# Optimization experiments

Hardware: AMD Instinct MI355X
Metric: run time of the kernel (lower is better)

The kernel has to match this reference:

```python
import jax, jax.numpy as jnp
import numpy as np

B, S, D, H = 4, 1024, 512, 8
EPS = 1e-5


def _cx(x):
    # [..., 2] float -> complex
    return jax.lax.complex(x[..., 0], x[..., 1])


def setup_inputs() -> dict:
    key = jax.random.key(0)
    ks = jax.random.split(key, 9)
    f = lambda k, sh: jax.random.normal(k, sh, dtype=jnp.float32)
    inp = {
        "q": f(ks[0], (B, S, D, 2)),
        "k": f(ks[1], (B, S, D, 2)),
        "v": f(ks[2], (B, S, D, 2)),
        "Wq": f(ks[3], (D, D, 2)) * 0.02,
        "bq": f(ks[4], (D, 2)) * 0.02,
        "Wk": f(ks[5], (D, D, 2)) * 0.02,
        "bk": f(ks[6], (D, 2)) * 0.02,
        "Wv": f(ks[7], (D, D, 2)) * 0.02,
        "bv": f(ks[8], (D, 2)) * 0.02,
        "gamma_r": jnp.ones((D,), jnp.float32),
        "beta_r": jnp.zeros((D,), jnp.float32),
        "gamma_i": jnp.ones((D,), jnp.float32),
        "beta_i": jnp.zeros((D,), jnp.float32),
        "n_heads": H,
    }
    return inp


def _layernorm(x, g, b):
    # torch LayerNorm: biased variance, eps inside sqrt
    mu = jnp.mean(x, axis=-1, keepdims=True)
    var = jnp.mean((x - mu) ** 2, axis=-1, keepdims=True)
    return (x - mu) / jnp.sqrt(var + EPS) * g + b


def reference(q, k, v, Wq, bq, Wk, bk, Wv, bv, gamma_r, beta_r, gamma_i, beta_i, n_heads):
    qc, kc, vc = _cx(q), _cx(k), _cx(v)
    # complex linear: x @ W^T + b
    Q = jnp.einsum("bsd,ed->bse", qc, _cx(Wq)) + _cx(bq)
    K = jnp.einsum("bsd,ed->bse", kc, _cx(Wk)) + _cx(bk)
    V = jnp.einsum("bsd,ed->bse", vc, _cx(Wv)) + _cx(bv)
    b, s, d = qc.shape
    dh = d // n_heads
    Qh = Q.reshape(b, s, n_heads, dh)
    Kh = K.reshape(b, s, n_heads, dh)
    Vh = V.reshape(b, s, n_heads, dh)
    # complex scores [b,h,q,k], scaled by sqrt(dh)
    scores = jnp.einsum("bqhd,bkhd->bhqk", Qh, Kh) / jnp.sqrt(jnp.float32(dh))
    # original: softmax over view_as_real dim=-2 == key axis, real & imag independently
    attn = jax.lax.complex(jax.nn.softmax(scores.real, axis=-1),
                           jax.nn.softmax(scores.imag, axis=-1))
    # (dropout is identity in eval mode)
    out = jnp.einsum("bhqk,bkhd->bqhd", attn, Vh).reshape(b, s, d)
    out = out + qc  # residual
    out_r = _layernorm(out.real, gamma_r, beta_r)
    out_i = _layernorm(out.imag, gamma_i, beta_i)
    return jnp.stack([out_r, out_i], axis=-1)  # [B,S,D,2]
```

## Files before the change

### kernel.cpp

```cpp
#include <hip/hip_runtime.h>
#include <math.h>

#define BB  4
#define SS  1024
#define DD  512
#define HH  8
#define DHD 64
#define PL  2097152
#define WPL 262144

constexpr float LN_EPS = 1e-5f;

using half4 = __attribute__((ext_vector_type(4))) _Float16;
using half8 = __attribute__((ext_vector_type(8))) _Float16;
using f32x4 = __attribute__((ext_vector_type(4))) float;

__device__ __forceinline__ half8 negh(half8 a) {
    union { half8 h; unsigned int u[4]; } t;
    t.h = a;
    #pragma unroll
    for (int i = 0; i < 4; ++i) t.u[i] ^= 0x80008000u;
    return t.h;
}
__device__ __forceinline__ half8 ldh64(const unsigned short* p, int row, int col) {
    return *(const half8*)(p + row * 64 + (col ^ ((row & 7) << 3)));
}
__device__ __forceinline__ unsigned int cvtpk(float a, float b) {
    union { decltype(__builtin_amdgcn_cvt_pkrtz(0.f, 0.f)) v; unsigned int u; } t;
    t.v = __builtin_amdgcn_cvt_pkrtz(a, b);
    return t.u;
}
__device__ __forceinline__ float ex2(float x) { return __builtin_amdgcn_exp2f(x); }
#define MFMA16(acc, a, b) acc = __builtin_amdgcn_mfma_f32_16x16x32_f16(a, b, acc, 0, 0, 0)

__global__ __launch_bounds__(256)
void cvt_kernel(const float2* __restrict__ s0, const float2* __restrict__ s1,
                const float2* __restrict__ s2, unsigned short* __restrict__ dst,
                int planeElems) {
    const int z = blockIdx.y;
    const float2* src = z == 0 ? s0 : (z == 1 ? s1 : s2);
    unsigned short* base = dst + (size_t)z * 2 * planeElems;
    const int idx = (blockIdx.x * 256 + threadIdx.x) * 2;
    float4 t = *(const float4*)(src + idx);
    const int m = idx >> 9;
    const int d = idx & 511;
    const int ob = (((m >> 7) << 3) + (d >> 6)) * 8192 + ((m & 127) << 6) + (d & 63);
    union { _Float16 h[2]; unsigned int u; } r, i;
    r.h[0] = (_Float16)t.x; r.h[1] = (_Float16)t.z;
    i.h[0] = (_Float16)t.y; i.h[1] = (_Float16)t.w;
    *(unsigned int*)(base + ob) = r.u;
    *(unsigned int*)(base + planeElems + ob) = i.u;
}

__global__ __launch_bounds__(256, 2)
void proj_kernel(const unsigned short* __restrict__ XP,
                 const unsigned short* __restrict__ WP,
                 const float2* __restrict__ bq, const float2* __restrict__ bk,
                 const float2* __restrict__ bv,
                 unsigned short* __restrict__ QG, unsigned short* __restrict__ KG,
                 unsigned short* __restrict__ VG) {
    const unsigned short* XR = XP + (size_t)blockIdx.z * 2 * PL;
    const unsigned short* XI = XR + PL;
    const unsigned short* WRp = WP + (size_t)blockIdx.z * 2 * WPL;
    const unsigned short* WIp = WRp + WPL;
    const float2* bias; unsigned short* outP;
    if (blockIdx.z == 0)      { bias = bq; outP = QG; }
    else if (blockIdx.z == 1) { bias = bk; outP = KG; }
    else                      { bias = bv; outP = VG; }
    const bool isV = (blockIdx.z == 2);

    __shared__ __align__(16) unsigned short Xs[2][128 * 64];
    __shared__ __align__(16) unsigned short Ws[2][128 * 64];

    const int tid  = threadIdx.x;
    const int w    = tid >> 6;
    const int lane = tid & 63;
    const int quad = lane >> 4;
    const int l15  = lane & 15;
    const int wm   = w >> 1;
    const int we   = w & 1;
    const int m0   = blockIdx.x * 128;
    const int e0   = blockIdx.y * 128;

    const int srow = lane >> 3;
    const int sg   = lane & 7;
    const unsigned short* gplane;
    unsigned short* lb;
    int row0;
    if (w == 0)      { gplane = XR;  row0 = m0; lb = &Xs[0][0]; }
    else if (w == 1) { gplane = XI;  row0 = m0; lb = &Xs[1][0]; }
    else if (w == 2) { gplane = WRp; row0 = e0; lb = &Ws[0][0]; }
    else             { gplane = WIp; row0 = e0; lb = &Ws[1][0]; }
    const unsigned short* gs = gplane + (size_t)row0 * DD + srow * 64 + ((sg ^ srow) << 3);

    f32x4 Sr[4][4], Si[4][4];
    #pragma unroll
    for (int a = 0; a < 4; ++a)
        #pragma unroll
        for (int c = 0; c < 4; ++c) { Sr[a][c] = (f32x4)0.f; Si[a][c] = (f32x4)0.f; }

    for (int s = 0; s < 8; ++s) {
        if (s) __syncthreads();
        const unsigned short* _g = gs + (size_t)s * 8192;
        #pragma unroll
        for (int j = 0; j < 16; ++j)
            __builtin_amdgcn_global_load_lds(
                (const __attribute__((address_space(1))) void*)(_g + j * 512),
                (__attribute__((address_space(3))) void*)(lb + j * 512),
                16, 0, 0);
        __syncthreads();

        #pragma unroll
        for (int kc = 0; kc < 2; ++kc) {
            const int dl = kc * 32 + quad * 8;
            half8 xr[4], xi[4];
            #pragma unroll
            for (int mf = 0; mf < 4; ++mf) {
                const int mr = wm * 64 + mf * 16 + l15;
                xr[mf] = ldh64(Xs[0], mr, dl);
                xi[mf] = ldh64(Xs[1], mr, dl);
            }
            #pragma unroll
            for (int ef = 0; ef < 4; ++ef) {
                const int er = we * 64 + ef * 16 + l15;
                half8 wr  = ldh64(Ws[0], er, dl);
                half8 wi  = ldh64(Ws[1], er, dl);
                half8 wmi = negh(wi);
                #pragma unroll
                for (int mf = 0; mf < 4; ++mf) {
                    MFMA16(Sr[mf][ef], xr[mf], wr);
                    MFMA16(Sr[mf][ef], xi[mf], wmi);
                    MFMA16(Si[mf][ef], xr[mf], wi);
                    MFMA16(Si[mf][ef], xi[mf], wr);
                }
            }
        }
    }

    #pragma unroll
    for (int ef = 0; ef < 4; ++ef) {
        const int eg  = e0 + we * 64 + ef * 16 + l15;
        const int hh  = eg >> 6;
        const int col = eg & 63;
        float2 bb = bias[eg];
        #pragma unroll
        for (int mf = 0; mf < 4; ++mf) {
            #pragma unroll
            for (int reg = 0; reg < 4; ++reg) {
                int m = m0 + wm * 64 + mf * 16 + quad * 4 + reg;
                int bidx = m >> 10;
                int sidx = m & 1023;
                int bh = bidx * HH + hh;
                union { _Float16 h; unsigned short u; } cr, ci;
                cr.h = (_Float16)(Sr[mf][ef][reg] + bb.x);
                ci.h = (_Float16)(Si[mf][ef][reg] + bb.y);
                size_t o = isV ? ((size_t)bh * DHD + col) * SS + sidx
                               : ((size_t)bh * SS + sidx) * DHD + col;
                outP[0 * PL + o] = cr.u;
                outP[1 * PL + o] = ci.u;
            }
        }
    }
}

#define AWID 72
__global__ __launch_bounds__(256, 2)
void attn_kernel(const unsigned short* __restrict__ QG, const unsigned short* __restrict__ KG,
                 const unsigned short* __restrict__ VG,
                 unsigned short* __restrict__ ObR, unsigned short* __restrict__ ObI) {
    __shared__ __align__(16) unsigned short Ks[2][2][64 * 64];
    __shared__ __align__(16) unsigned short Vt[2][64 * 64];
    __shared__ __align__(16) unsigned short Ps[2][64 * AWID];
    __shared__ float lbuf[2][2][64];

    const int n   = blockIdx.x;
    const int bh  = (n & 7) * 4 + (n >> 7);
    const int q0  = ((n >> 3) & 15) * 64;
    const int b   = bh >> 3;
    const int h   = bh & 7;

    const int tid  = threadIdx.x;
    const int w    = tid >> 6;
    const int lane = tid & 63;
    const int quad = lane >> 4;
    const int l15  = lane & 15;
    const int sw   = w & 1;
    const int tw   = w >> 1;

    const int srow = lane >> 3;
    const int sg   = lane & 7;
    const bool isK = (w < 2);
    const unsigned short* bpK = nullptr;
    const unsigned short* bpV = nullptr;
    unsigned short* ldV = nullptr;
    if (isK) {
        bpK = KG + (size_t)w * PL + (size_t)bh * SS * DHD + srow * DHD + ((sg ^ srow) << 3);
    } else {
        bpV = VG + (size_t)(w - 2) * PL + (size_t)bh * DHD * SS + srow * SS + ((sg ^ srow) << 3);
        ldV = &Vt[w - 2][0];
    }

#define GLD(SRC, DST) __builtin_amdgcn_global_load_lds( \
        (const __attribute__((address_space(1))) void*)(SRC), \
        (__attribute__((address_space(3))) void*)(DST), 16, 0, 0)

    if (isK) {
        unsigned short* ld = &Ks[0][w][0];
        #pragma unroll
        for (int j = 0; j < 8; ++j) GLD(bpK + j * 8 * DHD, ld + j * 512);
    }

    half8 qfr[2][2], qfi[2][2], qfmi[2][2];
    #pragma unroll
    for (int qt = 0; qt < 2; ++qt)
        #pragma unroll
        for (int kc = 0; kc < 2; ++kc) {
            size_t qa = ((size_t)bh * SS + q0 + sw * 32 + qt * 16 + l15) * DHD + kc * 32 + quad * 8;
            qfr[qt][kc]  = *(const half8*)(QG + qa);
            qfi[qt][kc]  = *(const half8*)(QG + PL + qa);
            qfmi[qt][kc] = negh(qfi[qt][kc]);
        }

    f32x4 acc[2][2][4];
    #pragma unroll
    for (int qt = 0; qt < 2; ++qt)
        #pragma unroll
        for (int dt = 0; dt < 2; ++dt)
            #pragma unroll
            for (int p = 0; p < 4; ++p) acc[qt][dt][p] = (f32x4)0.f;
    float lacc[2][2] = {{0.f, 0.f}, {0.f, 0.f}};

    constexpr float EC = 0.18033688011112042f;

    __syncthreads();

    const unsigned short* Kr_c = &Ks[0][0][0];
    const unsigned short* Ki_c = &Ks[0][1][0];
    const unsigned short* Kr_n = &Ks[1][0][0];
    const unsigned short* Ki_n = &Ks[1][1][0];
    unsigned short* kst_nxt = isK ? &Ks[1][w][0] : nullptr;
    unsigned short* kst_alt = isK ? &Ks[0][w][0] : nullptr;

    for (int t = 0; t < 16; ++t) {
        if (isK) {
            if (t < 15) {
                const unsigned short* g = bpK + (size_t)(t + 1) * 64 * DHD;
                #pragma unroll
                for (int j = 0; j < 8; ++j) GLD(g + j * 8 * DHD, kst_nxt + j * 512);
            }
        } else {
            const unsigned short* g = bpV + (size_t)t * 64;
            #pragma unroll
            for (int j = 0; j < 8; ++j) GLD(g + j * 8 * SS, ldV + j * 512);
        }

        f32x4 Sr[2][2], Si[2][2];
        #pragma unroll
        for (int a = 0; a < 2; ++a)
            #pragma unroll
            for (int c = 0; c < 2; ++c) { Sr[a][c] = (f32x4)0.f; Si[a][c] = (f32x4)0.f; }
        #pragma unroll
        for (int kc = 0; kc < 2; ++kc) {
            const int dl = kc * 32 + quad * 8;
            #pragma unroll
            for (int kt2 = 0; kt2 < 2; ++kt2) {
                const int krow = tw * 32 + kt2 * 16 + l15;
                half8 akr = ldh64(Kr_c, krow, dl);
                half8 aki = ldh64(Ki_c, krow, dl);
                #pragma unroll
                for (int qt = 0; qt < 2; ++qt) {
                    MFMA16(Sr[kt2][qt], akr, qfr[qt][kc]);
                    MFMA16(Sr[kt2][qt], aki, qfmi[qt][kc]);
                    MFMA16(Si[kt2][qt], aki, qfr[qt][kc]);
                    MFMA16(Si[kt2][qt], akr, qfi[qt][kc]);
                }
            }
        }

        #pragma unroll
        for (int kt2 = 0; kt2 < 2; ++kt2)
            #pragma unroll
            for (int qt = 0; qt < 2; ++qt) {
                float er0 = ex2(Sr[kt2][qt][0] * EC), er1 = ex2(Sr[kt2][qt][1] * EC);
                float er2 = ex2(Sr[kt2][qt][2] * EC), er3 = ex2(Sr[kt2][qt][3] * EC);
                float ei0 = ex2(Si[kt2][qt][0] * EC), ei1 = ex2(Si[kt2][qt][1] * EC);
                float ei2 = ex2(Si[kt2][qt][2] * EC), ei3 = ex2(Si[kt2][qt][3] * EC);
                lacc[qt][0] += (er0 + er1) + (er2 + er3);
                lacc[qt][1] += (ei0 + ei1) + (ei2 + ei3);
                const int qrow = sw * 32 + qt * 16 + l15;
                const int kcol = tw * 32 + kt2 * 16 + quad * 4;
                uint2 pr, pi;
                pr.x = cvtpk(er0, er1); pr.y = cvtpk(er2, er3);
                pi.x = cvtpk(ei0, ei1); pi.y = cvtpk(ei2, ei3);
                *(uint2*)&Ps[0][qrow * AWID + kcol] = pr;
                *(uint2*)&Ps[1][qrow * AWID + kcol] = pi;
            }
        __syncthreads();

        #pragma unroll
        for (int kc = 0; kc < 2; ++kc) {
            half8 ap[2][2];
            #pragma unroll
            for (int qt = 0; qt < 2; ++qt) {
                const int qrow = sw * 32 + qt * 16 + l15;
                ap[qt][0] = *(const half8*)&Ps[0][qrow * AWID + kc * 32 + quad * 8];
                ap[qt][1] = *(const half8*)&Ps[1][qrow * AWID + kc * 32 + quad * 8];
            }
            #pragma unroll
            for (int dt = 0; dt < 2; ++dt) {
                const int drow = tw * 32 + dt * 16 + l15;
                half8 bvr = ldh64(Vt[0], drow, kc * 32 + quad * 8);
                half8 bvi = ldh64(Vt[1], drow, kc * 32 + quad * 8);
                #pragma unroll
                for (int qt = 0; qt < 2; ++qt) {
                    MFMA16(acc[qt][dt][0], ap[qt][0], bvr);
                    MFMA16(acc[qt][dt][1], ap[qt][0], bvi);
                    MFMA16(acc[qt][dt][2], ap[qt][1], bvr);
                    MFMA16(acc[qt][dt][3], ap[qt][1], bvi);
                }
            }
        }
        __syncthreads();

        const unsigned short* tr;
        tr = Kr_c; Kr_c = Kr_n; Kr_n = tr;
        tr = Ki_c; Ki_c = Ki_n; Ki_n = tr;
        unsigned short* ts = kst_nxt; kst_nxt = kst_alt; kst_alt = ts;
    }
#undef GLD

    #pragma unroll
    for (int qt = 0; qt < 2; ++qt)
        #pragma unroll
        for (int p = 0; p < 2; ++p) {
            float v = lacc[qt][p];
            v += __shfl_xor(v, 16);
            v += __shfl_xor(v, 32);
            if (lane < 16) lbuf[p][tw][sw * 32 + qt * 16 + lane] = v;
        }
    __syncthreads();

    #pragma unroll
    for (int qt = 0; qt < 2; ++qt)
        #pragma unroll
        for (int reg = 0; reg < 4; ++reg) {
            const int qloc = sw * 32 + qt * 16 + quad * 4 + reg;
            const float ir = 1.f / (lbuf[0][0][qloc] + lbuf[0][1][qloc]);
            const float ii = 1.f / (lbuf[1][0][qloc] + lbuf[1][1][qloc]);
            #pragma unroll
            for (int dt = 0; dt < 2; ++dt) {
                const int d = tw * 32 + dt * 16 + l15;
                union { _Float16 h; unsigned short u; } cr, ci;
                cr.h = (_Float16)(acc[qt][dt][0][reg] * ir - acc[qt][dt][3][reg] * ii);
                ci.h = (_Float16)(acc[qt][dt][1][reg] * ir + acc[qt][dt][2][reg] * ii);
                size_t o = ((size_t)b * SS + q0 + qloc) * DD + h * DHD + d;
                ObR[o] = cr.u;
                ObI[o] = ci.u;
            }
        }
}

__global__ __launch_bounds__(256)
void ln_kernel(const unsigned short* __restrict__ OrP, const unsigned short* __restrict__ OiP,
               const float2* __restrict__ Qin,
               const float* __restrict__ gr, const float* __restrict__ br,
               const float* __restrict__ gi, const float* __restrict__ bi,
               float2* __restrict__ out) {
    const int row = blockIdx.x;
    const int tid = threadIdx.x;
    const size_t base = (size_t)row * DD;
    const int e0 = 2 * tid, e1 = 2 * tid + 1;

    union { unsigned int u; _Float16 h[2]; } tr, ti;
    tr.u = *(const unsigned int*)(OrP + base + e0);
    ti.u = *(const unsigned int*)(OiP + base + e0);
    float2 r0 = Qin[base + e0];
    float2 r1 = Qin[base + e1];
    float xr0 = (float)tr.h[0] + r0.x;
    float xr1 = (float)tr.h[1] + r1.x;
    float xi0 = (float)ti.h[0] + r0.y;
    float xi1 = (float)ti.h[1] + r1.y;

    float sr = xr0 + xr1;
    float si = xi0 + xi1;
    float qr = xr0 * xr0 + xr1 * xr1;
    float qi = xi0 * xi0 + xi1 * xi1;
    #pragma unroll
    for (int off = 32; off > 0; off >>= 1) {
        sr += __shfl_down(sr, off);
        si += __shfl_down(si, off);
        qr += __shfl_down(qr, off);
        qi += __shfl_down(qi, off);
    }
    __shared__ float red[4][4];
    __shared__ float stat[4];
    int lane = tid & 63, wid = tid >> 6;
    if (lane == 0) { red[wid][0] = sr; red[wid][1] = si; red[wid][2] = qr; red[wid][3] = qi; }
    __syncthreads();
    if (tid == 0) {
        sr = red[0][0] + red[1][0] + red[2][0] + red[3][0];
        si = red[0][1] + red[1][1] + red[2][1] + red[3][1];
        qr = red[0][2] + red[1][2] + red[2][2] + red[3][2];
        qi = red[0][3] + red[1][3] + red[2][3] + red[3][3];
        float mur = sr * (1.f / DD), mui = si * (1.f / DD);
        float vr = qr * (1.f / DD) - mur * mur;
        float vi = qi * (1.f / DD) - mui * mui;
        stat[0] = mur; stat[1] = mui;
        stat[2] = rsqrtf(vr + LN_EPS); stat[3] = rsqrtf(vi + LN_EPS);
    }
    __syncthreads();
    float mur = stat[0], mui = stat[1], rsr = stat[2], rsi = stat[3];
    out[base + e0] = make_float2((xr0 - mur) * rsr * gr[e0] + br[e0],
                                 (xi0 - mui) * rsi * gi[e0] + bi[e0]);
    out[base + e1] = make_float2((xr1 - mur) * rsr * gr[e1] + br[e1],
                                 (xi1 - mui) * rsi * gi[e1] + bi[e1]);
}

extern "C" void kernel_launch(void* const* d_in, const int* in_sizes, int n_in,
                              void* d_out, int out_size, void* d_ws, size_t ws_size,
                              hipStream_t stream) {
    const float2* q  = (const float2*)d_in[0];
    const float2* k  = (const float2*)d_in[1];
    const float2* v  = (const float2*)d_in[2];
    const float2* Wq = (const float2*)d_in[3];
    const float2* bq = (const float2*)d_in[4];
    const float2* Wk = (const float2*)d_in[5];
    const float2* bk = (const float2*)d_in[6];
    const float2* Wv = (const float2*)d_in[7];
    const float2* bv = (const float2*)d_in[8];
    const float*  gr = (const float*)d_in[9];
    const float*  br = (const float*)d_in[10];
    const float*  gi = (const float*)d_in[11];
    const float*  bi = (const float*)d_in[12];

    unsigned short* XP  = (unsigned short*)d_ws;
    unsigned short* WP  = XP + (size_t)6 * PL;
    unsigned short* QG  = WP + (size_t)6 * WPL;
    unsigned short* KG  = QG + (size_t)2 * PL;
    unsigned short* VG  = KG + (size_t)2 * PL;
    unsigned short* ObR = VG + (size_t)2 * PL;
    unsigned short* ObI = ObR + (size_t)PL;

    cvt_kernel<<<dim3(4096, 3), 256, 0, stream>>>(q, k, v, XP, PL);
    cvt_kernel<<<dim3(512, 3), 256, 0, stream>>>(Wq, Wk, Wv, WP, WPL);
    proj_kernel<<<dim3(32, 4, 3), 256, 0, stream>>>(XP, WP, bq, bk, bv, QG, KG, VG);
    attn_kernel<<<dim3(512), 256, 0, stream>>>(QG, KG, VG, ObR, ObI);
    ln_kernel<<<dim3(BB * SS), 256, 0, stream>>>(ObR, ObI, q, gr, br, gi, bi, (float2*)d_out);
}
```

Baseline: 205.2 us.

## Double-buffer projection LDS tiles and relax attention barriers with split waitcnts

The projection GEMM now loads K in 32-wide half-stages into two LDS buffers, so the global-to-LDS load of the next stage overlaps the MFMAs on the current one. This replaces the old load, full sync, compute pattern, and adds a new swizzled 32-column addressing helper. In the attention kernel, the __syncthreads calls are replaced by explicit s_waitcnt plus s_barrier, waiting on vector memory only where needed (isK), so in-flight loads are not drained too early. Both changes add more barriers per K step and rely on hand-written waitcnt correctness.

Result: slower. 209.3 us (+2.0%).

```diff
diff --git a/kernel.cpp b/kernel.cpp
--- a/kernel.cpp
+++ b/kernel.cpp
@@ -24,6 +24,11 @@
 }
 __device__ __forceinline__ half8 ldh64(const unsigned short* p, int row, int col) {
     return *(const half8*)(p + row * 64 + (col ^ ((row & 7) << 3)));
+}
+__device__ __forceinline__ half8 ldh32(const unsigned short* p, int r, int g2) {
+    const int R = r >> 1;
+    const int G = ((r & 1) << 2) | g2;
+    return *(const half8*)(p + R * 64 + ((G ^ (R & 7)) << 3));
 }
 __device__ __forceinline__ unsigned int cvtpk(float a, float b) {
     union { decltype(__builtin_amdgcn_cvt_pkrtz(0.f, 0.f)) v; unsigned int u; } t;
@@ -69,8 +74,8 @@
     else                      { bias = bv; outP = VG; }
     const bool isV = (blockIdx.z == 2);
 
-    __shared__ __align__(16) unsigned short Xs[2][128 * 64];
-    __shared__ __align__(16) unsigned short Ws[2][128 * 64];
+    __shared__ __align__(16) unsigned short Xs[2][2][64 * 64];
+    __shared__ __align__(16) unsigned short Ws[2][2][64 * 64];
 
     const int tid  = threadIdx.x;
     const int w    = tid >> 6;
@@ -82,16 +87,28 @@
     const int m0   = blockIdx.x * 128;
     const int e0   = blockIdx.y * 128;
 
-    const int srow = lane >> 3;
-    const int sg   = lane & 7;
+    const int srow8 = lane >> 3;
+    const int G     = (lane & 7) ^ srow8;
+    const int rl    = srow8 * 2 + (G >> 2);
+    const int g2s   = G & 3;
+
     const unsigned short* gplane;
-    unsigned short* lb;
+    unsigned short *lb0, *lb1;
     int row0;
-    if (w == 0)      { gplane = XR;  row0 = m0; lb = &Xs[0][0]; }
-    else if (w == 1) { gplane = XI;  row0 = m0; lb = &Xs[1][0]; }
-    else if (w == 2) { gplane = WRp; row0 = e0; lb = &Ws[0][0]; }
-    else             { gplane = WIp; row0 = e0; lb = &Ws[1][0]; }
-    const unsigned short* gs = gplane + (size_t)row0 * DD + srow * 64 + ((sg ^ srow) << 3);
+    if (w == 0)      { gplane = XR;  row0 = m0; lb0 = &Xs[0][0][0]; lb1 = &Xs[1][0][0]; }
+    else if (w == 1) { gplane = XI;  row0 = m0; lb0 = &Xs[0][1][0]; lb1 = &Xs[1][1][0]; }
+    else if (w == 2) { gplane = WRp; row0 = e0; lb0 = &Ws[0][0][0]; lb1 = &Ws[1][0][0]; }
+    else             { gplane = WIp; row0 = e0; lb0 = &Ws[0][1][0]; lb1 = &Ws[1][1][0]; }
+    const unsigned short* gsrc = gplane + (size_t)row0 * DD + rl * 64 + g2s * 8;
+
+#define PSTAGE(S, LB) { \
+        const unsigned short* _g = gsrc + ((S) >> 1) * 8192 + ((S) & 1) * 32; \
+        _Pragma("unroll") \
+        for (int j = 0; j < 8; ++j) \
+            __builtin_amdgcn_global_load_lds( \
+                (const __attribute__((address_space(1))) void*)(_g + j * 1024), \
+                (__attribute__((address_space(3))) void*)((LB) + j * 512), \
+                16, 0, 0); }
 
     f32x4 Sr[4][4], Si[4][4];
     #pragma unroll
@@ -99,43 +116,44 @@
         #pragma unroll
         for (int c = 0; c < 4; ++c) { Sr[a][c] = (f32x4)0.f; Si[a][c] = (f32x4)0.f; }
 
-    for (int s = 0; s < 8; ++s) {
-        if (s) __syncthreads();
-        const unsigned short* _g = gs + (size_t)s * 8192;
-        #pragma unroll
-        for (int j = 0; j < 16; ++j)
-            __builtin_amdgcn_global_load_lds(
-                (const __attribute__((address_space(1))) void*)(_g + j * 512),
-                (__attribute__((address_space(3))) void*)(lb + j * 512),
-                16, 0, 0);
-        __syncthreads();
-
-        #pragma unroll
-        for (int kc = 0; kc < 2; ++kc) {
-            const int dl = kc * 32 + quad * 8;
-            half8 xr[4], xi[4];
+    PSTAGE(0, lb0);
+    __syncthreads();
+
+    for (int s = 0; s < 16; ++s) {
+        const int bs = s & 1;
+        if (s < 15) PSTAGE(s + 1, bs ? lb0 : lb1);
+
+        const unsigned short* xb0 = &Xs[bs][0][0];
+        const unsigned short* xb1 = &Xs[bs][1][0];
+        const unsigned short* wb0 = &Ws[bs][0][0];
+        const unsigned short* wb1 = &Ws[bs][1][0];
+
+        half8 xr[4], xi[4];
+        #pragma unroll
+        for (int mf = 0; mf < 4; ++mf) {
+            const int mr = wm * 64 + mf * 16 + l15;
+            xr[mf] = ldh32(xb0, mr, quad);
+            xi[mf] = ldh32(xb1, mr, quad);
+        }
+        #pragma unroll
+        for (int ef = 0; ef < 4; ++ef) {
+            const int er = we * 64 + ef * 16 + l15;
+            half8 wr  = ldh32(wb0, er, quad);
+            half8 wi  = ldh32(wb1, er, quad);
+            half8 wmi = negh(wi);
             #pragma unroll
             for (int mf = 0; mf < 4; ++mf) {
-                const int mr = wm * 64 + mf * 16 + l15;
-                xr[mf] = ldh64(Xs[0], mr, dl);
-                xi[mf] = ldh64(Xs[1], mr, dl);
-            }
-            #pragma unroll
-            for (int ef = 0; ef < 4; ++ef) {
-                const int er = we * 64 + ef * 16 + l15;
-                half8 wr  = ldh64(Ws[0], er, dl);
-                half8 wi  = ldh64(Ws[1], er, dl);
-                half8 wmi = negh(wi);
-                #pragma unroll
-                for (int mf = 0; mf < 4; ++mf) {
-                    MFMA16(Sr[mf][ef], xr[mf], wr);
-                    MFMA16(Sr[mf][ef], xi[mf], wmi);
-                    MFMA16(Si[mf][ef], xr[mf], wi);
-                    MFMA16(Si[mf][ef], xi[mf], wr);
-                }
-            }
-        }
-    }
+                MFMA16(Sr[mf][ef], xr[mf], wr);
+                MFMA16(Sr[mf][ef], xi[mf], wmi);
+                MFMA16(Si[mf][ef], xr[mf], wi);
+                MFMA16(Si[mf][ef], xi[mf], wr);
+            }
+        }
+        asm volatile("s_waitcnt vmcnt(0)" ::: "memory");
+        __builtin_amdgcn_s_barrier();
+        asm volatile("" ::: "memory");
+    }
+#undef PSTAGE
 
     #pragma unroll
     for (int ef = 0; ef < 4; ++ef) {
@@ -295,7 +313,11 @@
                 *(uint2*)&Ps[0][qrow * AWID + kcol] = pr;
                 *(uint2*)&Ps[1][qrow * AWID + kcol] = pi;
             }
-        __syncthreads();
+
+        asm volatile("s_waitcnt lgkmcnt(0)" ::: "memory");
+        if (!isK) asm volatile("s_waitcnt vmcnt(0)" ::: "memory");
+        __builtin_amdgcn_s_barrier();
+        asm volatile("" ::: "memory");
 
         #pragma unroll
         for (int kc = 0; kc < 2; ++kc) {
@@ -320,7 +342,10 @@
                 }
             }
         }
-        __syncthreads();
+
+        if (isK) asm volatile("s_waitcnt vmcnt(0)" ::: "memory");
+        __builtin_amdgcn_s_barrier();
+        asm volatile("" ::: "memory");
 
         const unsigned short* tr;
         tr = Kr_c; Kr_c = Kr_n; Kr_n = tr;
```

## Halve projection M-tile to raise occupancy and relax attention barrier waits

Applied to the files above, without the earlier changes.

The projection kernel now uses 64-row M tiles instead of 128, doubling the grid and lowering accumulator registers so launch bounds can allow three blocks per CU. The global-to-LDS loads are reassigned so one wave loads both X planes and two waves load the weight planes, with the fourth wave idle during loads. Separately, the attention loop replaces full __syncthreads with explicit lgkmcnt/vmcnt waits plus s_barrier, placing the vmcnt wait differently for K-loading waves so prefetch loads can stay in flight across the P·V phase. The smaller tile reduces per-block reuse of the weight tile, and the hand-placed waits risk ordering errors if the load roles are misread.

New measurement: 205.9 us. Within noise of the previous version (+0.4%).

```diff
diff --git a/kernel.cpp b/kernel.cpp
--- a/kernel.cpp
+++ b/kernel.cpp
@@ -52,7 +52,7 @@
     *(unsigned int*)(base + planeElems + ob) = i.u;
 }
 
-__global__ __launch_bounds__(256, 2)
+__global__ __launch_bounds__(256, 3)
 void proj_kernel(const unsigned short* __restrict__ XP,
                  const unsigned short* __restrict__ WP,
                  const float2* __restrict__ bq, const float2* __restrict__ bk,
@@ -69,7 +69,7 @@
     else                      { bias = bv; outP = VG; }
     const bool isV = (blockIdx.z == 2);
 
-    __shared__ __align__(16) unsigned short Xs[2][128 * 64];
+    __shared__ __align__(16) unsigned short Xs[2][64 * 64];
     __shared__ __align__(16) unsigned short Ws[2][128 * 64];
 
     const int tid  = threadIdx.x;
@@ -79,44 +79,55 @@
     const int l15  = lane & 15;
     const int wm   = w >> 1;
     const int we   = w & 1;
-    const int m0   = blockIdx.x * 128;
+    const int m0   = blockIdx.x * 64;
     const int e0   = blockIdx.y * 128;
 
-    const int srow = lane >> 3;
-    const int sg   = lane & 7;
-    const unsigned short* gplane;
-    unsigned short* lb;
-    int row0;
-    if (w == 0)      { gplane = XR;  row0 = m0; lb = &Xs[0][0]; }
-    else if (w == 1) { gplane = XI;  row0 = m0; lb = &Xs[1][0]; }
-    else if (w == 2) { gplane = WRp; row0 = e0; lb = &Ws[0][0]; }
-    else             { gplane = WIp; row0 = e0; lb = &Ws[1][0]; }
-    const unsigned short* gs = gplane + (size_t)row0 * DD + srow * 64 + ((sg ^ srow) << 3);
-
-    f32x4 Sr[4][4], Si[4][4];
-    #pragma unroll
-    for (int a = 0; a < 4; ++a)
+    const int srow8 = lane >> 3;
+    const int sg    = lane & 7;
+    const int swz   = ((sg ^ srow8) << 3);
+    const int xbase = ((m0 >> 7) << 16) + ((m0 & 127) << 6);
+    const int wbase = ((e0 >> 7) << 16);
+    const unsigned short* gsX  = XR  + xbase + srow8 * 64 + swz;
+    const unsigned short* gsW0 = WRp + wbase + srow8 * 64 + swz;
+    const unsigned short* gsW1 = WIp + wbase + srow8 * 64 + swz;
+
+#define GLD(SRC, DST) __builtin_amdgcn_global_load_lds( \
+        (const __attribute__((address_space(1))) void*)(SRC), \
+        (__attribute__((address_space(3))) void*)(DST), 16, 0, 0)
+
+    f32x4 Sr[2][4], Si[2][4];
+    #pragma unroll
+    for (int a = 0; a < 2; ++a)
         #pragma unroll
         for (int c = 0; c < 4; ++c) { Sr[a][c] = (f32x4)0.f; Si[a][c] = (f32x4)0.f; }
 
     for (int s = 0; s < 8; ++s) {
         if (s) __syncthreads();
-        const unsigned short* _g = gs + (size_t)s * 8192;
-        #pragma unroll
-        for (int j = 0; j < 16; ++j)
-            __builtin_amdgcn_global_load_lds(
-                (const __attribute__((address_space(1))) void*)(_g + j * 512),
-                (__attribute__((address_space(3))) void*)(lb + j * 512),
-                16, 0, 0);
+        if (w == 0) {
+            const unsigned short* g = gsX + s * 8192;
+            #pragma unroll
+            for (int jj = 0; jj < 16; ++jj)
+                GLD(g + (jj >> 3) * PL + (jj & 7) * 512, &Xs[jj >> 3][(jj & 7) * 512]);
+        } else if (w == 1) {
+            const unsigned short* g = gsW0 + s * 8192;
+            #pragma unroll
+            for (int jj = 0; jj < 16; ++jj)
+                GLD(g + jj * 512, &Ws[0][jj * 512]);
+        } else if (w == 2) {
+            const unsigned short* g = gsW1 + s * 8192;
+            #pragma unroll
+            for (int jj = 0; jj < 16; ++jj)
+                GLD(g + jj * 512, &Ws[1][jj * 512]);
+        }
         __syncthreads();
 
         #pragma unroll
         for (int kc = 0; kc < 2; ++kc) {
             const int dl = kc * 32 + quad * 8;
-            half8 xr[4], xi[4];
-            #pragma unroll
-            for (int mf = 0; mf < 4; ++mf) {
-                const int mr = wm * 64 + mf * 16 + l15;
+            half8 xr[2], xi[2];
+            #pragma unroll
+            for (int mf = 0; mf < 2; ++mf) {
+                const int mr = wm * 32 + mf * 16 + l15;
                 xr[mf] = ldh64(Xs[0], mr, dl);
                 xi[mf] = ldh64(Xs[1], mr, dl);
             }
@@ -127,7 +138,7 @@
                 half8 wi  = ldh64(Ws[1], er, dl);
                 half8 wmi = negh(wi);
                 #pragma unroll
-                for (int mf = 0; mf < 4; ++mf) {
+                for (int mf = 0; mf < 2; ++mf) {
                     MFMA16(Sr[mf][ef], xr[mf], wr);
                     MFMA16(Sr[mf][ef], xi[mf], wmi);
                     MFMA16(Si[mf][ef], xr[mf], wi);
@@ -136,6 +147,7 @@
             }
         }
     }
+#undef GLD
 
     #pragma unroll
     for (int ef = 0; ef < 4; ++ef) {
@@ -144,10 +156,10 @@
         const int col = eg & 63;
         float2 bb = bias[eg];
         #pragma unroll
-        for (int mf = 0; mf < 4; ++mf) {
+        for (int mf = 0; mf < 2; ++mf) {
             #pragma unroll
             for (int reg = 0; reg < 4; ++reg) {
-                int m = m0 + wm * 64 + mf * 16 + quad * 4 + reg;
+                int m = m0 + wm * 32 + mf * 16 + quad * 4 + reg;
                 int bidx = m >> 10;
                 int sidx = m & 1023;
                 int bh = bidx * HH + hh;
@@ -295,7 +307,11 @@
                 *(uint2*)&Ps[0][qrow * AWID + kcol] = pr;
                 *(uint2*)&Ps[1][qrow * AWID + kcol] = pi;
             }
-        __syncthreads();
+
+        asm volatile("s_waitcnt lgkmcnt(0)" ::: "memory");
+        if (!isK) asm volatile("s_waitcnt vmcnt(0)" ::: "memory");
+        __builtin_amdgcn_s_barrier();
+        asm volatile("" ::: "memory");
 
         #pragma unroll
         for (int kc = 0; kc < 2; ++kc) {
@@ -320,7 +336,10 @@
                 }
             }
         }
-        __syncthreads();
+
+        if (isK) asm volatile("s_waitcnt vmcnt(0)" ::: "memory");
+        __builtin_amdgcn_s_barrier();
+        asm volatile("" ::: "memory");
 
         const unsigned short* tr;
         tr = Kr_c; Kr_c = Kr_n; Kr_n = tr;
@@ -443,7 +462,7 @@
 
     cvt_kernel<<<dim3(4096, 3), 256, 0, stream>>>(q, k, v, XP, PL);
     cvt_kernel<<<dim3(512, 3), 256, 0, stream>>>(Wq, Wk, Wv, WP, WPL);
-    proj_kernel<<<dim3(32, 4, 3), 256, 0, stream>>>(XP, WP, bq, bk, bv, QG, KG, VG);
+    proj_kernel<<<dim3(64, 4, 3), 256, 0, stream>>>(XP, WP, bq, bk, bv, QG, KG, VG);
     attn_kernel<<<dim3(512), 256, 0, stream>>>(QG, KG, VG, ObR, ObI);
     ln_kernel<<<dim3(BB * SS), 256, 0, stream>>>(ObR, ObI, q, gr, br, gi, bi, (float2*)d_out);
 }
```
